# Optimization experiments

Measured on AMD Instinct MI355X. Metric: run time of the kernel, lower is better.

The kernel has to match this reference:

```python
import jax, jax.numpy as jnp
import numpy as np

B, L, C, D = 4, 2048, 64, 4


def setup_inputs() -> dict:
    key = jax.random.key(0)
    k1, k2, k3, k4 = jax.random.split(key, 4)
    # |A| kept < ~0.92 so the length-2048 recurrence stays bounded
    A_re = jax.random.uniform(k1, (B, L, C, D), jnp.float32, -0.65, 0.65)
    A_im = jax.random.uniform(k2, (B, L, C, D), jnp.float32, -0.65, 0.65)
    X_re = jax.random.normal(k3, (B, L, C, D, D), jnp.float32)
    X_im = jax.random.normal(k4, (B, L, C, D, D), jnp.float32)
    return {"A_re": A_re, "A_im": A_im, "X_re": X_re, "X_im": X_im}


def _combine(c1, c2):
    # first-order linear recurrence combine: (a, x) o (b, y) = (b*a, b*x + y)
    a1, x1 = c1
    a2, x2 = c2
    return a2 * a1, a2 * x1 + x2


def reference(A_re, A_im, X_re, X_im):
    # Diagonal complex pscan: Y[t] = A[t] * Y[t-1] + X[t], elementwise,
    # with diagonal A [B,L,C,D] broadcast over the trailing D dim of X [B,L,C,D,D]
    A = (A_re + 1j * A_im).astype(jnp.complex64)[..., None]  # [B,L,C,D,1]
    X = (X_re + 1j * X_im).astype(jnp.complex64)             # [B,L,C,D,D]
    _, Y = jax.lax.associative_scan(_combine, (A, X), axis=1)
    # return real view [B,L,C,D,D,2] (real, imag) like torch.view_as_real
    return jnp.stack([Y.real, Y.imag], axis=-1)
```

## Files before the change

kernel.cpp:

```cpp
#include <hip/hip_runtime.h>

#define BB 4
#define LL 2048
#define CC 64
#define DD 4
#define NN (CC * DD * DD)
#define GG 32
#define TT (LL / GG)


__global__ __launch_bounds__(256) void pscan_phase1(
    const float* __restrict__ A_re, const float* __restrict__ A_im,
    const float* __restrict__ X_re, const float* __restrict__ X_im,
    float4* __restrict__ agg) {
  int u = blockIdx.x * 256 + threadIdx.x;
  int n  = u & (NN - 1);
  int bg = u >> 10;
  int g  = bg & (GG - 1);
  int b  = bg >> 5;
  int t0 = g * TT;
  long baseA = (long)(b * LL + t0) * (CC * DD) + (n >> 2);
  long baseX = (long)(b * LL + t0) * NN + n;

  float p_re = 1.f, p_im = 0.f, s_re = 0.f, s_im = 0.f;
#pragma unroll 8
  for (int t = 0; t < TT; ++t) {
    float are = A_re[baseA + (long)t * (CC * DD)];
    float aim = A_im[baseA + (long)t * (CC * DD)];
    float xre = X_re[baseX + (long)t * NN];
    float xim = X_im[baseX + (long)t * NN];
    float nsre = are * s_re - aim * s_im + xre;
    float nsim = are * s_im + aim * s_re + xim;
    float npre = are * p_re - aim * p_im;
    float npim = are * p_im + aim * p_re;
    s_re = nsre; s_im = nsim; p_re = npre; p_im = npim;
  }
  agg[u] = make_float4(p_re, p_im, s_re, s_im);
}

__global__ __launch_bounds__(256) void pscan_phase2(float4* __restrict__ agg) {
  int u = blockIdx.x * 256 + threadIdx.x;
  int n = u & (NN - 1);
  int b = u >> 10;
  float rp_re = 1.f, rp_im = 0.f, rs_re = 0.f, rs_im = 0.f;
  for (int g = 0; g < GG; ++g) {
    long idx = (long)(b * GG + g) * NN + n;
    float4 v = agg[idx];
    agg[idx] = make_float4(rp_re, rp_im, rs_re, rs_im);
    float np_re = v.x * rp_re - v.y * rp_im;
    float np_im = v.x * rp_im + v.y * rp_re;
    float ns_re = v.x * rs_re - v.y * rs_im + v.z;
    float ns_im = v.x * rs_im + v.y * rs_re + v.w;
    rp_re = np_re; rp_im = np_im; rs_re = ns_re; rs_im = ns_im;
  }
}

__global__ __launch_bounds__(256) void pscan_phase3(
    const float* __restrict__ A_re, const float* __restrict__ A_im,
    const float* __restrict__ X_re, const float* __restrict__ X_im,
    const float4* __restrict__ carry, float2* __restrict__ out) {
  int u = blockIdx.x * 256 + threadIdx.x;
  int n  = u & (NN - 1);
  int bg = u >> 10;
  int g  = bg & (GG - 1);
  int b  = bg >> 5;
  int t0 = g * TT;
  long baseA = (long)(b * LL + t0) * (CC * DD) + (n >> 2);
  long baseX = (long)(b * LL + t0) * NN + n;

  float4 cv = carry[u];
  float y_re = cv.z, y_im = cv.w;
#pragma unroll 8
  for (int t = 0; t < TT; ++t) {
    float are = A_re[baseA + (long)t * (CC * DD)];
    float aim = A_im[baseA + (long)t * (CC * DD)];
    float xre = X_re[baseX + (long)t * NN];
    float xim = X_im[baseX + (long)t * NN];
    float ny_re = are * y_re - aim * y_im + xre;
    float ny_im = are * y_im + aim * y_re + xim;
    y_re = ny_re; y_im = ny_im;
    out[baseX + (long)t * NN] = make_float2(y_re, y_im);
  }
}

extern "C" void kernel_launch(void* const* d_in, const int* in_sizes, int n_in,
                              void* d_out, int out_size, void* d_ws, size_t ws_size,
                              hipStream_t stream) {
  const float* A_re = (const float*)d_in[0];
  const float* A_im = (const float*)d_in[1];
  const float* X_re = (const float*)d_in[2];
  const float* X_im = (const float*)d_in[3];
  float2* out = (float2*)d_out;
  float4* agg = (float4*)d_ws;

  const int total = BB * GG * NN;
  pscan_phase1<<<total / 256, 256, 0, stream>>>(A_re, A_im, X_re, X_im, agg);
  pscan_phase2<<<(BB * NN) / 256, 256, 0, stream>>>(agg);
  pscan_phase3<<<total / 256, 256, 0, stream>>>(A_re, A_im, X_re, X_im, agg, out);
}
```

Baseline: 156.4 us.

## Vectorize scan over D with float4 loads and add two-level carry propagation

Each thread now handles four X elements that share one diagonal A value, using 128-bit loads and nontemporal 128-bit stores, so A loads are shared and memory transactions widen. The chunk count grows from 32 to 128 to keep enough threads busy. The serial carry scan is split into a segmented phase 2a and a top-level phase 2b, and phase 3 folds the two carries together at startup. The cost is an extra kernel launch and more workspace traffic for the larger aggregate buffer.

Result: slower. 182.9 us (+16.9%).

```diff
diff --git a/kernel.cpp b/kernel.cpp
--- a/kernel.cpp
+++ b/kernel.cpp
@@ -5,81 +5,152 @@
 #define CC 64
 #define DD 4
 #define NN (CC * DD * DD)
-#define GG 32
+#define AN (CC * DD)
+#define GG 128
 #define TT (LL / GG)
+#define SEGLEN 16
+#define NSEG (GG / SEGLEN)
+
+typedef float f32x4 __attribute__((ext_vector_type(4)));
 
 
 __global__ __launch_bounds__(256) void pscan_phase1(
     const float* __restrict__ A_re, const float* __restrict__ A_im,
-    const float* __restrict__ X_re, const float* __restrict__ X_im,
-    float4* __restrict__ agg) {
-  int u = blockIdx.x * 256 + threadIdx.x;
-  int n  = u & (NN - 1);
-  int bg = u >> 10;
+    const f32x4* __restrict__ X_re4, const f32x4* __restrict__ X_im4,
+    f32x4* __restrict__ agg) {
+  int u  = blockIdx.x * 256 + threadIdx.x;
+  int n4 = u & (AN - 1);
+  int bg = u >> 8;
   int g  = bg & (GG - 1);
-  int b  = bg >> 5;
+  int b  = bg >> 7;
   int t0 = g * TT;
-  long baseA = (long)(b * LL + t0) * (CC * DD) + (n >> 2);
-  long baseX = (long)(b * LL + t0) * NN + n;
+  int baseA = (b * LL + t0) * AN + n4;
+  int baseX = (b * LL + t0) * AN + n4;
 
-  float p_re = 1.f, p_im = 0.f, s_re = 0.f, s_im = 0.f;
+  float p_re = 1.f, p_im = 0.f;
+  float s_re[4] = {0.f, 0.f, 0.f, 0.f};
+  float s_im[4] = {0.f, 0.f, 0.f, 0.f};
+
 #pragma unroll 8
   for (int t = 0; t < TT; ++t) {
-    float are = A_re[baseA + (long)t * (CC * DD)];
-    float aim = A_im[baseA + (long)t * (CC * DD)];
-    float xre = X_re[baseX + (long)t * NN];
-    float xim = X_im[baseX + (long)t * NN];
-    float nsre = are * s_re - aim * s_im + xre;
-    float nsim = are * s_im + aim * s_re + xim;
+    float are = A_re[baseA + t * AN];
+    float aim = A_im[baseA + t * AN];
+    f32x4 xr  = X_re4[baseX + t * AN];
+    f32x4 xi  = X_im4[baseX + t * AN];
     float npre = are * p_re - aim * p_im;
     float npim = are * p_im + aim * p_re;
-    s_re = nsre; s_im = nsim; p_re = npre; p_im = npim;
+    p_re = npre; p_im = npim;
+#pragma unroll
+    for (int j = 0; j < 4; ++j) {
+      float nsre = are * s_re[j] - aim * s_im[j] + xr[j];
+      float nsim = are * s_im[j] + aim * s_re[j] + xi[j];
+      s_re[j] = nsre; s_im[j] = nsim;
+    }
   }
-  agg[u] = make_float4(p_re, p_im, s_re, s_im);
+  int ab = (b * GG + g) * NN + n4 * 4;
+#pragma unroll
+  for (int j = 0; j < 4; ++j) {
+    f32x4 v = {p_re, p_im, s_re[j], s_im[j]};
+    agg[ab + j] = v;
+  }
 }
 
-__global__ __launch_bounds__(256) void pscan_phase2(float4* __restrict__ agg) {
+__global__ __launch_bounds__(256) void pscan_phase2a(
+    f32x4* __restrict__ agg, f32x4* __restrict__ segAgg) {
+  int u   = blockIdx.x * 256 + threadIdx.x;
+  int n   = u & (NN - 1);
+  int r   = u >> 10;
+  int seg = r & (NSEG - 1);
+  int b   = r >> 3;
+  int base = (b * GG + seg * SEGLEN) * NN + n;
+
+  f32x4 v[SEGLEN];
+#pragma unroll
+  for (int t = 0; t < SEGLEN; ++t) v[t] = agg[base + t * NN];
+
+  float rp_re = 1.f, rp_im = 0.f, rs_re = 0.f, rs_im = 0.f;
+#pragma unroll
+  for (int t = 0; t < SEGLEN; ++t) {
+    f32x4 cur = v[t];
+    f32x4 run = {rp_re, rp_im, rs_re, rs_im};
+    agg[base + t * NN] = run;
+    float np_re = cur.x * rp_re - cur.y * rp_im;
+    float np_im = cur.x * rp_im + cur.y * rp_re;
+    float ns_re = cur.x * rs_re - cur.y * rs_im + cur.z;
+    float ns_im = cur.x * rs_im + cur.y * rs_re + cur.w;
+    rp_re = np_re; rp_im = np_im; rs_re = ns_re; rs_im = ns_im;
+  }
+  f32x4 tot = {rp_re, rp_im, rs_re, rs_im};
+  segAgg[(b * NSEG + seg) * NN + n] = tot;
+}
+
+__global__ __launch_bounds__(256) void pscan_phase2b(f32x4* __restrict__ segAgg) {
   int u = blockIdx.x * 256 + threadIdx.x;
   int n = u & (NN - 1);
   int b = u >> 10;
+  int base = b * NSEG * NN + n;
+
+  f32x4 v[NSEG];
+#pragma unroll
+  for (int s = 0; s < NSEG; ++s) v[s] = segAgg[base + s * NN];
+
   float rp_re = 1.f, rp_im = 0.f, rs_re = 0.f, rs_im = 0.f;
-  for (int g = 0; g < GG; ++g) {
-    long idx = (long)(b * GG + g) * NN + n;
-    float4 v = agg[idx];
-    agg[idx] = make_float4(rp_re, rp_im, rs_re, rs_im);
-    float np_re = v.x * rp_re - v.y * rp_im;
-    float np_im = v.x * rp_im + v.y * rp_re;
-    float ns_re = v.x * rs_re - v.y * rs_im + v.z;
-    float ns_im = v.x * rs_im + v.y * rs_re + v.w;
+#pragma unroll
+  for (int s = 0; s < NSEG; ++s) {
+    f32x4 cur = v[s];
+    f32x4 run = {rp_re, rp_im, rs_re, rs_im};
+    segAgg[base + s * NN] = run;
+    float np_re = cur.x * rp_re - cur.y * rp_im;
+    float np_im = cur.x * rp_im + cur.y * rp_re;
+    float ns_re = cur.x * rs_re - cur.y * rs_im + cur.z;
+    float ns_im = cur.x * rs_im + cur.y * rs_re + cur.w;
     rp_re = np_re; rp_im = np_im; rs_re = ns_re; rs_im = ns_im;
   }
 }
 
 __global__ __launch_bounds__(256) void pscan_phase3(
     const float* __restrict__ A_re, const float* __restrict__ A_im,
-    const float* __restrict__ X_re, const float* __restrict__ X_im,
-    const float4* __restrict__ carry, float2* __restrict__ out) {
-  int u = blockIdx.x * 256 + threadIdx.x;
-  int n  = u & (NN - 1);
-  int bg = u >> 10;
+    const f32x4* __restrict__ X_re4, const f32x4* __restrict__ X_im4,
+    const f32x4* __restrict__ agg, const f32x4* __restrict__ segAgg,
+    f32x4* __restrict__ out4) {
+  int u  = blockIdx.x * 256 + threadIdx.x;
+  int n4 = u & (AN - 1);
+  int bg = u >> 8;
   int g  = bg & (GG - 1);
-  int b  = bg >> 5;
+  int b  = bg >> 7;
   int t0 = g * TT;
-  long baseA = (long)(b * LL + t0) * (CC * DD) + (n >> 2);
-  long baseX = (long)(b * LL + t0) * NN + n;
+  int seg = g >> 4;
+  int baseA = (b * LL + t0) * AN + n4;
+  int baseX = (b * LL + t0) * AN + n4;
+  int ab = (b * GG + g) * NN + n4 * 4;
+  int sb = (b * NSEG + seg) * NN + n4 * 4;
 
-  float4 cv = carry[u];
-  float y_re = cv.z, y_im = cv.w;
+  float y_re[4], y_im[4];
+#pragma unroll
+  for (int j = 0; j < 4; ++j) {
+    f32x4 la = agg[ab + j];
+    f32x4 sa = segAgg[sb + j];
+    y_re[j] = la.x * sa.z - la.y * sa.w + la.z;
+    y_im[j] = la.x * sa.w + la.y * sa.z + la.w;
+  }
+
+  int ob = (b * LL + t0) * (2 * AN) + n4 * 2;
 #pragma unroll 8
   for (int t = 0; t < TT; ++t) {
-    float are = A_re[baseA + (long)t * (CC * DD)];
-    float aim = A_im[baseA + (long)t * (CC * DD)];
-    float xre = X_re[baseX + (long)t * NN];
-    float xim = X_im[baseX + (long)t * NN];
-    float ny_re = are * y_re - aim * y_im + xre;
-    float ny_im = are * y_im + aim * y_re + xim;
-    y_re = ny_re; y_im = ny_im;
-    out[baseX + (long)t * NN] = make_float2(y_re, y_im);
+    float are = A_re[baseA + t * AN];
+    float aim = A_im[baseA + t * AN];
+    f32x4 xr  = X_re4[baseX + t * AN];
+    f32x4 xi  = X_im4[baseX + t * AN];
+#pragma unroll
+    for (int j = 0; j < 4; ++j) {
+      float ny_re = are * y_re[j] - aim * y_im[j] + xr[j];
+      float ny_im = are * y_im[j] + aim * y_re[j] + xi[j];
+      y_re[j] = ny_re; y_im[j] = ny_im;
+    }
+    f32x4 o0 = {y_re[0], y_im[0], y_re[1], y_im[1]};
+    f32x4 o1 = {y_re[2], y_im[2], y_re[3], y_im[3]};
+    __builtin_nontemporal_store(o0, &out4[ob + t * (2 * AN)]);
+    __builtin_nontemporal_store(o1, &out4[ob + t * (2 * AN) + 1]);
   }
 }
 
@@ -88,13 +159,16 @@
                               hipStream_t stream) {
   const float* A_re = (const float*)d_in[0];
   const float* A_im = (const float*)d_in[1];
-  const float* X_re = (const float*)d_in[2];
-  const float* X_im = (const float*)d_in[3];
-  float2* out = (float2*)d_out;
-  float4* agg = (float4*)d_ws;
+  const f32x4* X_re4 = (const f32x4*)d_in[2];
+  const f32x4* X_im4 = (const f32x4*)d_in[3];
+  f32x4* out4 = (f32x4*)d_out;
 
-  const int total = BB * GG * NN;
-  pscan_phase1<<<total / 256, 256, 0, stream>>>(A_re, A_im, X_re, X_im, agg);
-  pscan_phase2<<<(BB * NN) / 256, 256, 0, stream>>>(agg);
-  pscan_phase3<<<total / 256, 256, 0, stream>>>(A_re, A_im, X_re, X_im, agg, out);
+  f32x4* agg    = (f32x4*)d_ws;
+  f32x4* segAgg = (f32x4*)((char*)d_ws + (size_t)BB * GG * NN * 16);
+
+  const int total = BB * GG * AN;
+  pscan_phase1<<<total / 256, 256, 0, stream>>>(A_re, A_im, X_re4, X_im4, agg);
+  pscan_phase2a<<<(BB * NSEG * NN) / 256, 256, 0, stream>>>(agg, segAgg);
+  pscan_phase2b<<<(BB * NN) / 256, 256, 0, stream>>>(segAgg);
+  pscan_phase3<<<total / 256, 256, 0, stream>>>(A_re, A_im, X_re4, X_im4, agg, segAgg, out4);
 }
```
